# Performance work log

Hardware: AMD Instinct MI355X
Metric: run time of the kernel (lower is better)

The kernel has to match this reference:

```python
import jax, jax.numpy as jnp
import numpy as np

N_NODES = 32768
NUM_EDGES = 524288
NUM_GRAPHS = 32
C = 128            # hidden channels
N_LAYERS = 3       # len(hidden_channels)-1
D_IN = 144         # 4 (op embedding dim) + 140
C_MID = 80         # mem1 out
C_OUT = 64         # mem2 out / classes
H1, K1N = 5, 10    # mem1 heads / clusters
H2, K2N = 5, 1     # mem2 heads / clusters
EPS = 1e-15


def _gatv2(x, src, dst, Wl, bl, Wr, br, att, cb):
    """GATv2Conv (heads=1, negative_slope=0.2), edges src->dst incl. self loops."""
    n = x.shape[0]
    xl = x @ Wl + bl                                  # source transform [N,C]
    xr = x @ Wr + br                                  # target transform [N,C]
    e = (jax.nn.leaky_relu(xl[src] + xr[dst], 0.2) @ att)  # [E]
    m = jax.ops.segment_max(e, dst, num_segments=n)   # segment softmax over in-edges
    ee = jnp.exp(e - m[dst])
    denom = jax.ops.segment_sum(ee, dst, num_segments=n)
    alpha = ee / denom[dst]
    out = jax.ops.segment_sum(alpha[:, None] * xl[src], dst, num_segments=n)
    return out + cb


def _bn(h, gamma, beta):
    # BatchNorm1d with batch statistics (training-mode forward), eps=1e-5
    mu = h.mean(0)
    var = h.var(0)
    return (h - mu) * jax.lax.rsqrt(var + 1e-5) * gamma + beta


def _mem_pool(xd, Kmem, W):
    # xd [B,N,C], Kmem [H,K,C]; Student-t kernel, tau=1 -> (1+d)^-1
    d = (jnp.sum(xd * xd, -1)[:, :, None, None]
         + jnp.sum(Kmem * Kmem, -1)[None, None]
         - 2.0 * jnp.einsum('bnc,hkc->bnhk', xd, Kmem))  # [B,N,H,K] sq. distances
    S = 1.0 / (1.0 + d)
    S = S / S.sum(-1, keepdims=True)   # normalize over clusters
    S = S.mean(2)                      # average heads -> [B,N,K]
    out = jnp.einsum('bnk,bnc->bkc', S, xd) @ W
    return out, S


def _kl_loss(S):
    S2 = S * S / S.sum(1, keepdims=True)
    den = S2.sum(2, keepdims=True)
    den = jnp.where(S.sum(2, keepdims=True) == 0.0, 1.0, den)
    P = jnp.maximum(S2 / den, EPS)
    Sc = jnp.maximum(S, EPS)
    # KLDivLoss(reduction='batchmean'), input = log(S)
    return jnp.sum(P * (jnp.log(P) - jnp.log(Sc))) / S.shape[0]


def setup_inputs():
    key = jax.random.key(0)
    ks = jax.random.split(key, 24)
    x = jax.random.normal(ks[0], (N_NODES, D_IN), jnp.float32)
    edge_index = jax.random.randint(ks[1], (2, NUM_EDGES), 0, N_NODES, jnp.int32)
    batch = (jnp.arange(N_NODES, dtype=jnp.int32) // (N_NODES // NUM_GRAPHS))
    s = 1.0 / np.sqrt(C)
    inp = {
        'x': x, 'edge_index': edge_index, 'batch': batch,
        'W_in': jax.random.normal(ks[2], (D_IN, C), jnp.float32) / np.sqrt(D_IN),
        'b_in': jnp.zeros((C,), jnp.float32),
        'bn_gamma': jnp.ones((N_LAYERS, C), jnp.float32),
        'bn_beta': jnp.zeros((N_LAYERS, C), jnp.float32),
        'Wl': jax.random.normal(ks[3], (N_LAYERS, C, C), jnp.float32) * s,
        'bl': jnp.zeros((N_LAYERS, C), jnp.float32),
        'Wr': jax.random.normal(ks[4], (N_LAYERS, C, C), jnp.float32) * s,
        'br': jnp.zeros((N_LAYERS, C), jnp.float32),
        'att': jax.random.normal(ks[5], (N_LAYERS, C), jnp.float32) * s,
        'conv_bias': jnp.zeros((N_LAYERS, C), jnp.float32),
        'K1': jax.random.normal(ks[6], (H1, K1N, C), jnp.float32),
        'Wm1': jax.random.normal(ks[7], (C, C_MID), jnp.float32) * s,
        'K2': jax.random.normal(ks[8], (H2, K2N, C_MID), jnp.float32),
        'Wm2': jax.random.normal(ks[9], (C_MID, C_OUT), jnp.float32) / np.sqrt(C_MID),
    }
    return inp


def reference(x, edge_index, batch, W_in, b_in, bn_gamma, bn_beta,
              Wl, bl, Wr, br, att, conv_bias, K1, Wm1, K2, Wm2):
    h = x @ W_in + b_in                               # self.linear
    loops = jnp.arange(N_NODES, dtype=edge_index.dtype)
    src = jnp.concatenate([edge_index[0], loops])     # GATv2 add_self_loops=True
    dst = jnp.concatenate([edge_index[1], loops])
    for l in range(N_LAYERS):                         # DeepGCNLayer block='res+'
        t = _bn(h, bn_gamma[l], bn_beta[l])
        t = jax.nn.leaky_relu(t, 0.01)
        # dropout: identity (deterministic reference)
        t = _gatv2(t, src, dst, Wl[l], bl[l], Wr[l], br[l], att[l], conv_bias[l])
        h = h + t
    per = N_NODES // NUM_GRAPHS
    xd = h.reshape(NUM_GRAPHS, per, C)                # to_dense_batch (equal-size graphs)
    x1, S1 = _mem_pool(xd, K1, Wm1)                   # [B,10,80]
    x1 = jax.nn.leaky_relu(x1, 0.01)
    x2, S2 = _mem_pool(x1, K2, Wm2)                   # [B,1,64]
    logits = jax.nn.log_softmax(x2.squeeze(1), -1)    # [B,64]
    return logits, _kl_loss(S1) + _kl_loss(S2)
```

## Files before the change

kernel.cpp:

```cpp
#include <hip/hip_runtime.h>
#include <math.h>

#define N_NODES   32768
#define NUM_EDGES 524288
#define NUM_GRAPHS 32
#define PER_G     1024
#define C         128
#define D_IN      144
#define C_MID     80
#define C_OUT     64
#define NL        3
#define NBINS     32

#define WS_H    0
#define WS_XL   16777216
#define WS_XR   25165824
#define WS_CSR  33554432
#define WS_DEG  35651584
#define WS_CUR  35782656
#define WS_PART 35913728
#define WS_CS   35946496
#define WS_KL   35947776
#define WS_ZERO_BASE WS_DEG
#define WS_ZERO_SIZE (35947780 - 35651584)
#define WS_SC   35948544
#define WS_SH   35949056
#define WS_S1   35949568
#define WS_PP   37260288
#define WS_X1   42503168
#define WS_OFF  42605568

using short8 = __attribute__((ext_vector_type(8))) short;
using f32x4  = __attribute__((ext_vector_type(4))) float;

__device__ __forceinline__ float wave_sum(float v) {
  #pragma unroll
  for (int m = 1; m < 64; m <<= 1) v += __shfl_xor(v, m, 64);
  return v;
}

__device__ __forceinline__ float lrelu2(float v) { return fmaxf(v, 0.2f * v); }

__device__ __forceinline__ unsigned short f2bf(float f) {
  union { float f; unsigned u; } c; c.f = f;
  unsigned r = (c.u + 0x7FFFu + ((c.u >> 16) & 1u)) >> 16;
  return (unsigned short)r;
}
__device__ __forceinline__ float bflo(unsigned u) {
  union { unsigned u; float f; } c; c.u = u << 16; return c.f;
}
__device__ __forceinline__ float bfhi(unsigned u) {
  union { unsigned u; float f; } c; c.u = u & 0xFFFF0000u; return c.f;
}

__global__ void k_count(const int* __restrict__ dst, int* __restrict__ deg) {
  int e = blockIdx.x * 256 + threadIdx.x;
  if (e < NUM_EDGES) atomicAdd(&deg[dst[e]], 1);
}

__global__ __launch_bounds__(1024) void k_scan(const int* __restrict__ deg, int* __restrict__ off) {
  __shared__ int part[1024];
  int t = threadIdx.x;
  int base = t * 32;
  int4 d[8];
  const int4* dp = (const int4*)(deg + base);
  #pragma unroll
  for (int i = 0; i < 8; i++) d[i] = dp[i];
  int s = 0;
  #pragma unroll
  for (int i = 0; i < 8; i++) s += d[i].x + d[i].y + d[i].z + d[i].w;
  part[t] = s;
  __syncthreads();
  for (int dd = 1; dd < 1024; dd <<= 1) {
    int v = (t >= dd) ? part[t - dd] : 0;
    __syncthreads();
    part[t] += v;
    __syncthreads();
  }
  int run = (t == 0) ? 0 : part[t - 1];
  int4* op = (int4*)(off + base);
  #pragma unroll
  for (int i = 0; i < 8; i++) {
    int4 o;
    o.x = run; run += d[i].x;
    o.y = run; run += d[i].y;
    o.z = run; run += d[i].z;
    o.w = run; run += d[i].w;
    op[i] = o;
  }
}

__global__ void k_fill(const int* __restrict__ src, const int* __restrict__ dst,
                       const int* __restrict__ off, int* __restrict__ cur,
                       int* __restrict__ csr) {
  int e = blockIdx.x * 256 + threadIdx.x;
  if (e < NUM_EDGES) {
    int d = dst[e];
    int p = atomicAdd(&cur[d], 1);
    csr[off[d] + p] = src[e];
  }
}

__global__ __launch_bounds__(256) void k_lin_mfma(const float* __restrict__ x,
    const float* __restrict__ W, const float* __restrict__ bias,
    float* __restrict__ h, float* __restrict__ part) {
  __shared__ __align__(16) char smem[61440];
  __shared__ float lsum[128];
  __shared__ float lsum2[128];
  char* tA = smem;
  char* tB = smem + 20480;
  int n0 = blockIdx.x * 64;
  int tid = threadIdx.x;
  if (tid < 128) { lsum[tid] = 0.f; lsum2[tid] = 0.f; }
  for (int t = 0; t < 32; t++) {
    int cp = tid & 127;
    int node = t * 2 + (tid >> 7);
    if (cp < 80) {
      unsigned pkv = 0;
      if (cp < 72) {
        float2 xv = *(const float2*)&x[(size_t)(n0 + node) * D_IN + 2 * cp];
        pkv = ((unsigned)f2bf(xv.y) << 16) | f2bf(xv.x);
      }
      int byte = node * 320 + ((4 * cp) ^ ((node & 3) << 4));
      *(unsigned*)(tA + byte) = pkv;
    }
  }
  {
    int col = tid & 127, hh = tid >> 7;
    for (int t = 0; t < 40; t++) {
      int kp = t * 2 + hh;
      float w0 = (2 * kp < D_IN) ? W[(size_t)(2 * kp) * C + col] : 0.f;
      float w1 = (2 * kp + 1 < D_IN) ? W[(size_t)(2 * kp + 1) * C + col] : 0.f;
      unsigned pkv = ((unsigned)f2bf(w1) << 16) | f2bf(w0);
      int byte = col * 320 + ((4 * kp) ^ ((col & 3) << 4));
      *(unsigned*)(tB + byte) = pkv;
    }
  }
  __syncthreads();
  int l = tid & 63, w = tid >> 6;
  f32x4 acc[8];
  #pragma unroll
  for (int f = 0; f < 8; f++) acc[f] = (f32x4){0.f, 0.f, 0.f, 0.f};
  int arow = w * 16 + (l & 15);
  #pragma unroll
  for (int ks = 0; ks < 5; ks++) {
    int kb = ks * 64 + (l >> 4) * 16;
    short8 a = *(const short8*)(tA + arow * 320 + (kb ^ ((arow & 3) << 4)));
    #pragma unroll
    for (int f = 0; f < 8; f++) {
      int col = f * 16 + (l & 15);
      short8 b = *(const short8*)(tB + col * 320 + (kb ^ ((col & 3) << 4)));
      acc[f] = __builtin_amdgcn_mfma_f32_16x16x32_bf16(a, b, acc[f], 0, 0, 0);
    }
  }
  int rowb = n0 + w * 16 + (l >> 4) * 4;
  #pragma unroll
  for (int f = 0; f < 8; f++) {
    int col = f * 16 + (l & 15);
    float bv = bias[col];
    float s = 0.f, s2 = 0.f;
    #pragma unroll
    for (int r = 0; r < 4; r++) {
      float v = acc[f][r] + bv;
      h[(size_t)(rowb + r) * C + col] = v;
      s += v; s2 += v * v;
    }
    s  += __shfl_xor(s, 16, 64);  s  += __shfl_xor(s, 32, 64);
    s2 += __shfl_xor(s2, 16, 64); s2 += __shfl_xor(s2, 32, 64);
    if (l < 16) {
      atomicAdd(&lsum[col], s);
      atomicAdd(&lsum2[col], s2);
    }
  }
  __syncthreads();
  if (tid < 128) {
    int bin = blockIdx.x & (NBINS - 1);
    atomicAdd(&part[bin * 256 + tid], lsum[tid]);
    atomicAdd(&part[bin * 256 + 128 + tid], lsum2[tid]);
  }
}

__global__ __launch_bounds__(128) void k_bn_part(const float* __restrict__ h, float* __restrict__ part) {
  int b = blockIdx.x; int c = threadIdx.x;
  float s = 0.f, s2 = 0.f;
  int r0 = b * 64;
  for (int r = 0; r < 64; r++) {
    float v = h[(size_t)(r0 + r) * C + c];
    s += v; s2 += v * v;
  }
  int bin = b & (NBINS - 1);
  atomicAdd(&part[bin * 256 + c], s);
  atomicAdd(&part[bin * 256 + 128 + c], s2);
}

__global__ __launch_bounds__(256) void k_bn_fin(float* __restrict__ part,
    const float* __restrict__ gamma, const float* __restrict__ beta,
    float* __restrict__ sc, float* __restrict__ sh) {
  int tid = threadIdx.x;
  if (tid < 128) {
    double S = 0.0, S2 = 0.0;
    for (int b = 0; b < NBINS; b++) {
      S += (double)part[b * 256 + tid];
      S2 += (double)part[b * 256 + 128 + tid];
    }
    double m = S / (double)N_NODES;
    double var = S2 / (double)N_NODES - m * m;
    float rsig = (float)(1.0 / sqrt(var + 1e-5));
    float scv = rsig * gamma[tid];
    sc[tid] = scv;
    sh[tid] = beta[tid] - (float)m * scv;
  }
  __syncthreads();
  for (int i = tid; i < NBINS * 256; i += 256) part[i] = 0.f;
}

__device__ __forceinline__ void gemm_half(const char* tA, const char* tB,
    const float* bias, unsigned short* out, int n0, int tid) {
  int l = tid & 63, w = tid >> 6;
  f32x4 acc[8];
  #pragma unroll
  for (int f = 0; f < 8; f++) acc[f] = (f32x4){0.f, 0.f, 0.f, 0.f};
  int arow = w * 16 + (l & 15);
  #pragma unroll
  for (int ks = 0; ks < 4; ks++) {
    int kb = ks * 64 + (l >> 4) * 16;
    short8 a = *(const short8*)(tA + arow * 256 + (kb ^ ((arow & 7) << 4)));
    #pragma unroll
    for (int f = 0; f < 8; f++) {
      int col = f * 16 + (l & 15);
      short8 b = *(const short8*)(tB + col * 256 + (kb ^ ((col & 7) << 4)));
      acc[f] = __builtin_amdgcn_mfma_f32_16x16x32_bf16(a, b, acc[f], 0, 0, 0);
    }
  }
  int rowb = n0 + w * 16 + (l >> 4) * 4;
  #pragma unroll
  for (int f = 0; f < 8; f++) {
    int col = f * 16 + (l & 15);
    float bv = bias[col];
    #pragma unroll
    for (int r = 0; r < 4; r++)
      out[(size_t)(rowb + r) * C + col] = f2bf(acc[f][r] + bv);
  }
}

__device__ __forceinline__ void stage_B(char* tB, const float* __restrict__ W, int tid) {
  int col = tid & 127, hh = tid >> 7;
  for (int t = 0; t < 32; t++) {
    int kp = t * 2 + hh;
    float w0 = W[(size_t)(2 * kp) * C + col];
    float w1 = W[(size_t)(2 * kp + 1) * C + col];
    unsigned pkv = ((unsigned)f2bf(w1) << 16) | f2bf(w0);
    int byte = col * 256 + ((4 * kp) ^ ((col & 7) << 4));
    *(unsigned*)(tB + byte) = pkv;
  }
}

__global__ __launch_bounds__(256) void k_gemm_mfma(const float* __restrict__ h,
    const float* __restrict__ sc, const float* __restrict__ sh,
    const float* __restrict__ Wl, const float* __restrict__ bl,
    const float* __restrict__ Wr, const float* __restrict__ br,
    unsigned short* __restrict__ xl, unsigned short* __restrict__ xr) {
  __shared__ __align__(16) char smem[49152];
  char* tA = smem;
  char* tB = smem + 16384;
  int n0 = blockIdx.x * 64;
  int tid = threadIdx.x;
  for (int t = 0; t < 16; t++) {
    int item = t * 256 + tid;
    int node = item >> 6;
    int cp = item & 63;
    float2 hv = *(const float2*)&h[(size_t)(n0 + node) * C + 2 * cp];
    float2 scv = *(const float2*)&sc[2 * cp];
    float2 shv = *(const float2*)&sh[2 * cp];
    float t0 = hv.x * scv.x + shv.x; t0 = fmaxf(t0, 0.01f * t0);
    float t1 = hv.y * scv.y + shv.y; t1 = fmaxf(t1, 0.01f * t1);
    unsigned pkv = ((unsigned)f2bf(t1) << 16) | f2bf(t0);
    int byte = node * 256 + ((4 * cp) ^ ((node & 7) << 4));
    *(unsigned*)(tA + byte) = pkv;
  }
  stage_B(tB, Wl, tid);
  __syncthreads();
  gemm_half(tA, tB, bl, xl, n0, tid);
  __syncthreads();
  stage_B(tB, Wr, tid);
  __syncthreads();
  gemm_half(tA, tB, br, xr, n0, tid);
}

#define GAT_EDGE(te, ya, yb, yc, yd)                                       \
  if ((te) > m + 8.f) {                                                    \
    float f_ = __expf(m - (te));                                           \
    ssum = fmaf(ssum, f_, 1.f);                                            \
    acc0 = fmaf(acc0, f_, (ya)); acc1 = fmaf(acc1, f_, (yb));              \
    acc2 = fmaf(acc2, f_, (yc)); acc3 = fmaf(acc3, f_, (yd));              \
    m = (te);                                                              \
  } else {                                                                 \
    float p_ = __expf((te) - m);                                           \
    ssum += p_;                                                            \
    acc0 = fmaf(p_, (ya), acc0); acc1 = fmaf(p_, (yb), acc1);              \
    acc2 = fmaf(p_, (yc), acc2); acc3 = fmaf(p_, (yd), acc3);              \
  }

__global__ __launch_bounds__(256) void k_gat(float* __restrict__ h,
    const unsigned* __restrict__ xlb, const unsigned* __restrict__ xrb,
    const float* __restrict__ att, const float* __restrict__ cb,
    const int* __restrict__ off, const int* __restrict__ deg,
    const int* __restrict__ csr) {
  int tid = threadIdx.x;
  int lane = tid & 63;
  int w = tid >> 6;
  int half = lane >> 5;
  int q = lane & 31;
  int node = blockIdx.x * 8 + w * 2 + half;
  float4 a = *(const float4*)&att[q * 4];
  uint2 ur = *(const uint2*)&xrb[(size_t)node * 64 + q * 2];
  float xr0 = bflo(ur.x), xr1 = bfhi(ur.x), xr2 = bflo(ur.y), xr3 = bfhi(ur.y);
  uint2 us = *(const uint2*)&xlb[(size_t)node * 64 + q * 2];
  float acc0 = bflo(us.x), acc1 = bfhi(us.x), acc2 = bflo(us.y), acc3 = bfhi(us.y);
  float p0 = lrelu2(acc0 + xr0) * a.x + lrelu2(acc1 + xr1) * a.y
           + lrelu2(acc2 + xr2) * a.z + lrelu2(acc3 + xr3) * a.w;
  #pragma unroll
  for (int mm = 1; mm < 32; mm <<= 1) p0 += __shfl_xor(p0, mm, 64);
  float m = p0;
  float ssum = 1.f;
  int o = off[node], dg = deg[node];
  int dgmax = max(dg, __shfl_xor(dg, 32, 64));
  for (int j = 0; j < dgmax; j += 4) {
    int i0 = o + ((j + 0 < dg) ? j + 0 : 0);
    int i1 = o + ((j + 1 < dg) ? j + 1 : 0);
    int i2 = o + ((j + 2 < dg) ? j + 2 : 0);
    int i3 = o + ((j + 3 < dg) ? j + 3 : 0);
    int s0 = csr[i0], s1 = csr[i1], s2 = csr[i2], s3 = csr[i3];
    uint2 u0 = *(const uint2*)&xlb[(size_t)s0 * 64 + q * 2];
    uint2 u1 = *(const uint2*)&xlb[(size_t)s1 * 64 + q * 2];
    uint2 u2 = *(const uint2*)&xlb[(size_t)s2 * 64 + q * 2];
    uint2 u3 = *(const uint2*)&xlb[(size_t)s3 * 64 + q * 2];
    float y00 = bflo(u0.x), y01 = bfhi(u0.x), y02 = bflo(u0.y), y03 = bfhi(u0.y);
    float y10 = bflo(u1.x), y11 = bfhi(u1.x), y12 = bflo(u1.y), y13 = bfhi(u1.y);
    float y20 = bflo(u2.x), y21 = bfhi(u2.x), y22 = bflo(u2.y), y23 = bfhi(u2.y);
    float y30 = bflo(u3.x), y31 = bfhi(u3.x), y32 = bflo(u3.y), y33 = bfhi(u3.y);
    float t0 = lrelu2(y00 + xr0) * a.x + lrelu2(y01 + xr1) * a.y
             + lrelu2(y02 + xr2) * a.z + lrelu2(y03 + xr3) * a.w;
    float t1 = lrelu2(y10 + xr0) * a.x + lrelu2(y11 + xr1) * a.y
             + lrelu2(y12 + xr2) * a.z + lrelu2(y13 + xr3) * a.w;
    float t2 = lrelu2(y20 + xr0) * a.x + lrelu2(y21 + xr1) * a.y
             + lrelu2(y22 + xr2) * a.z + lrelu2(y23 + xr3) * a.w;
    float t3 = lrelu2(y30 + xr0) * a.x + lrelu2(y31 + xr1) * a.y
             + lrelu2(y32 + xr2) * a.z + lrelu2(y33 + xr3) * a.w;
    #pragma unroll
    for (int mm = 1; mm < 32; mm <<= 1) {
      t0 += __shfl_xor(t0, mm, 64);
      t1 += __shfl_xor(t1, mm, 64);
      t2 += __shfl_xor(t2, mm, 64);
      t3 += __shfl_xor(t3, mm, 64);
    }
    t0 = (j + 0 < dg) ? t0 : -1e30f;
    t1 = (j + 1 < dg) ? t1 : -1e30f;
    t2 = (j + 2 < dg) ? t2 : -1e30f;
    t3 = (j + 3 < dg) ? t3 : -1e30f;
    GAT_EDGE(t0, y00, y01, y02, y03);
    GAT_EDGE(t1, y10, y11, y12, y13);
    GAT_EDGE(t2, y20, y21, y22, y23);
    GAT_EDGE(t3, y30, y31, y32, y33);
  }
  float inv = 1.f / ssum;
  float4 cbv = *(const float4*)&cb[q * 4];
  float4 hv = *(float4*)&h[(size_t)node * C + q * 4];
  hv.x += acc0 * inv + cbv.x;
  hv.y += acc1 * inv + cbv.y;
  hv.z += acc2 * inv + cbv.z;
  hv.w += acc3 * inv + cbv.w;
  *(float4*)&h[(size_t)node * C + q * 4] = hv;
}

__global__ __launch_bounds__(320) void k_mem1(const float* __restrict__ h,
    const float* __restrict__ K1, float* __restrict__ S1, float* __restrict__ colsum) {
  __shared__ float dd[64 * 51];
  __shared__ float kn[50];
  int tid = threadIdx.x;
  int lane = tid & 63;
  int w = tid >> 6;
  int n0 = blockIdx.x * 64;
  if (tid < 50) {
    const float4* kr = reinterpret_cast<const float4*>(K1 + tid * C);
    float s = 0.f;
    for (int q = 0; q < 32; q++) {
      float4 kv = kr[q];
      s += kv.x * kv.x + kv.y * kv.y + kv.z * kv.z + kv.w * kv.w;
    }
    kn[tid] = s;
  }
  int wu = __builtin_amdgcn_readfirstlane(w);
  const float4* x4 = reinterpret_cast<const float4*>(h + (size_t)(n0 + lane) * C);
  const float4* K4 = reinterpret_cast<const float4*>(K1);
  float acc[10];
  #pragma unroll
  for (int it = 0; it < 10; it++) acc[it] = 0.f;
  float xn = 0.f;
  for (int q = 0; q < 32; q += 2) {
    float4 xa = x4[q], xb = x4[q + 1];
    xn += xa.x * xa.x + xa.y * xa.y + xa.z * xa.z + xa.w * xa.w
        + xb.x * xb.x + xb.y * xb.y + xb.z * xb.z + xb.w * xb.w;
    #pragma unroll
    for (int it = 0; it < 10; it++) {
      int j = wu + 5 * it;
      float4 ka = K4[j * 32 + q], kb = K4[j * 32 + q + 1];
      acc[it] += xa.x * ka.x + xa.y * ka.y + xa.z * ka.z + xa.w * ka.w
               + xb.x * kb.x + xb.y * kb.y + xb.z * kb.z + xb.w * kb.w;
    }
  }
  #pragma unroll
  for (int it = 0; it < 10; it++) dd[lane * 51 + wu + 5 * it] = acc[it];
  __syncthreads();
  if (tid < 64) {
    float sn[10];
    #pragma unroll
    for (int k = 0; k < 10; k++) sn[k] = 0.f;
    #pragma unroll
    for (int hd = 0; hd < 5; hd++) {
      float sh_[10]; float hs = 0.f;
      #pragma unroll
      for (int k = 0; k < 10; k++) {
        int j = hd * 10 + k;
        float dist = xn + kn[j] - 2.f * dd[tid * 51 + j];
        float s = 1.f / (1.f + dist);
        sh_[k] = s; hs += s;
      }
      float inv = 1.f / hs;
      #pragma unroll
      for (int k = 0; k < 10; k++) sn[k] += sh_[k] * inv;
    }
    int b = n0 >> 10;
    #pragma unroll
    for (int k = 0; k < 10; k++) {
      float v = 0.2f * sn[k];
      S1[(n0 + tid) * 10 + k] = v;
      float vs = wave_sum(v);
      if (tid == 0) atomicAdd(&colsum[b * 10 + k], vs);
    }
  }
}

__global__ __launch_bounds__(128) void k_pool1a(const float* __restrict__ h,
    const float* __restrict__ S1, float* __restrict__ pp) {
  int b = blockIdx.x >> 5, ch = blockIdx.x & 31;
  int c = threadIdx.x;
  float acc[10];
  #pragma unroll
  for (int k = 0; k < 10; k++) acc[k] = 0.f;
  int n0 = ch * 32;
  for (int n = 0; n < 32; n++) {
    int i = b * PER_G + n0 + n;
    float xv = h[(size_t)i * C + c];
    #pragma unroll
    for (int k = 0; k < 10; k++) acc[k] += S1[i * 10 + k] * xv;
  }
  #pragma unroll
  for (int k = 0; k < 10; k++) pp[(size_t)((b * 32 + ch) * 10 + k) * C + c] = acc[k];
}

__global__ __launch_bounds__(128) void k_pool1b(const float* __restrict__ pp,
    const float* __restrict__ Wm1, float* __restrict__ x1) {
  int bk = blockIdx.x; int b = bk / 10; int k = bk - b * 10;
  int c = threadIdx.x;
  __shared__ float red[C];
  float r = 0.f;
  for (int ch = 0; ch < 32; ch++) r += pp[(size_t)((b * 32 + ch) * 10 + k) * C + c];
  red[c] = r;
  __syncthreads();
  if (c < C_MID) {
    float o = 0.f;
    for (int mIdx = 0; mIdx < C; mIdx++) o += red[mIdx] * Wm1[mIdx * C_MID + c];
    o = fmaxf(o, 0.01f * o);
    x1[bk * C_MID + c] = o;
  }
}

__global__ __launch_bounds__(256) void k_kl1(const float* __restrict__ S1,
    const float* __restrict__ colsum, float* __restrict__ kl) {
  int i = blockIdx.x * 256 + threadIdx.x;
  int b = i >> 10;
  float s[10], q[10];
  float den = 0.f;
  #pragma unroll
  for (int k = 0; k < 10; k++) {
    s[k] = S1[i * 10 + k];
    q[k] = s[k] * s[k] / colsum[b * 10 + k];
    den += q[k];
  }
  float inv = 1.f / den;
  float term = 0.f;
  #pragma unroll
  for (int k = 0; k < 10; k++) {
    float P = fmaxf(q[k] * inv, 1e-15f);
    float Sc = fmaxf(s[k], 1e-15f);
    term += P * (logf(P) - logf(Sc));
  }
  term *= (1.f / (float)NUM_GRAPHS);
  term = wave_sum(term);
  if ((threadIdx.x & 63) == 0) atomicAdd(kl, term);
}

__global__ __launch_bounds__(128) void k_mem2(const float* __restrict__ x1,
    const float* __restrict__ Wm2, const float* __restrict__ kl, float* __restrict__ out) {
  int b = blockIdx.x;
  __shared__ float t80[C_MID];
  int tid = threadIdx.x;
  if (tid < C_MID) {
    float s = 0.f;
    #pragma unroll
    for (int k = 0; k < 10; k++) s += x1[(b * 10 + k) * C_MID + tid];
    t80[tid] = s;
  }
  __syncthreads();
  if (tid < C_OUT) {
    float o = 0.f;
    for (int mIdx = 0; mIdx < C_MID; mIdx++) o += t80[mIdx] * Wm2[mIdx * C_OUT + tid];
    float mx = o;
    #pragma unroll
    for (int d = 1; d < 64; d <<= 1) mx = fmaxf(mx, __shfl_xor(mx, d, 64));
    float p = expf(o - mx);
    float sum = p;
    #pragma unroll
    for (int d = 1; d < 64; d <<= 1) sum += __shfl_xor(sum, d, 64);
    out[b * C_OUT + tid] = o - mx - logf(sum);
  }
  if (b == 0 && tid == 127) out[NUM_GRAPHS * C_OUT] = kl[0];
}

extern "C" void kernel_launch(void* const* d_in, const int* in_sizes, int n_in,
                              void* d_out, int out_size, void* d_ws, size_t ws_size,
                              hipStream_t stream) {
  const float* x    = (const float*)d_in[0];
  const int*   ei   = (const int*)d_in[1];
  const float* W_in = (const float*)d_in[3];
  const float* b_in = (const float*)d_in[4];
  const float* bn_g = (const float*)d_in[5];
  const float* bn_b = (const float*)d_in[6];
  const float* Wl   = (const float*)d_in[7];
  const float* bl   = (const float*)d_in[8];
  const float* Wr   = (const float*)d_in[9];
  const float* br   = (const float*)d_in[10];
  const float* att  = (const float*)d_in[11];
  const float* cb   = (const float*)d_in[12];
  const float* K1   = (const float*)d_in[13];
  const float* Wm1  = (const float*)d_in[14];
  const float* Wm2  = (const float*)d_in[16];
  float* out = (float*)d_out;

  char* ws = (char*)d_ws;
  float* h    = (float*)(ws + WS_H);
  unsigned short* xlp = (unsigned short*)(ws + WS_XL);
  unsigned short* xrp = (unsigned short*)(ws + WS_XR);
  int*   csr  = (int*)(ws + WS_CSR);
  int*   deg  = (int*)(ws + WS_DEG);
  int*   off  = (int*)(ws + WS_OFF);
  int*   cur  = (int*)(ws + WS_CUR);
  float* part = (float*)(ws + WS_PART);
  float* scv  = (float*)(ws + WS_SC);
  float* shv  = (float*)(ws + WS_SH);
  float* S1p  = (float*)(ws + WS_S1);
  float* cs   = (float*)(ws + WS_CS);
  float* pp   = (float*)(ws + WS_PP);
  float* x1p  = (float*)(ws + WS_X1);
  float* klp  = (float*)(ws + WS_KL);

  const int* srcp = ei;
  const int* dstp = ei + NUM_EDGES;

  hipMemsetAsync(ws + WS_ZERO_BASE, 0, WS_ZERO_SIZE, stream);

  k_count<<<NUM_EDGES / 256, 256, 0, stream>>>(dstp, deg);
  k_scan<<<1, 1024, 0, stream>>>(deg, off);
  k_fill<<<NUM_EDGES / 256, 256, 0, stream>>>(srcp, dstp, off, cur, csr);

  k_lin_mfma<<<N_NODES / 64, 256, 0, stream>>>(x, W_in, b_in, h, part);

  for (int l = 0; l < NL; l++) {
    if (l > 0) k_bn_part<<<N_NODES / 64, 128, 0, stream>>>(h, part);
    k_bn_fin<<<1, 256, 0, stream>>>(part, bn_g + l * C, bn_b + l * C, scv, shv);
    k_gemm_mfma<<<N_NODES / 64, 256, 0, stream>>>(h, scv, shv,
        Wl + l * C * C, bl + l * C,
        Wr + l * C * C, br + l * C,
        xlp, xrp);
    k_gat<<<N_NODES / 8, 256, 0, stream>>>(h, (const unsigned*)xlp, (const unsigned*)xrp,
        att + l * C, cb + l * C, off, deg, csr);
  }

  k_mem1<<<N_NODES / 64, 320, 0, stream>>>(h, K1, S1p, cs);
  k_pool1a<<<NUM_GRAPHS * 32, 128, 0, stream>>>(h, S1p, pp);
  k_pool1b<<<NUM_GRAPHS * 10, 128, 0, stream>>>(pp, Wm1, x1p);
  k_kl1<<<N_NODES / 256, 256, 0, stream>>>(S1p, cs, klp);
  k_mem2<<<NUM_GRAPHS, 128, 0, stream>>>(x1p, Wm2, klp, out);
}
```

Baseline: 303.5 us.

## Pre-pack bf16 swizzled weights once and vectorize GEMM tile staging

Adds a prep kernel that converts W_in, Wl and Wr to bf16 in the swizzled shared-memory layout once per call, so each GEMM block copies the B tile with 16-byte loads instead of re-converting strided fp32 weights. The A-tile staging in the input linear now uses float4 loads with a changed swizzle, and the GEMM A staging batches its loads before converting. This removes redundant per-block weight conversion in exchange for one extra small launch and more workspace.

```diff
diff --git a/kernel.cpp b/kernel.cpp
--- a/kernel.cpp
+++ b/kernel.cpp
@@ -29,6 +29,8 @@
 #define WS_PP   37260288
 #define WS_X1   42503168
 #define WS_OFF  42605568
+#define WS_WINT 42736640
+#define WS_WLRT 42777600
 
 using short8 = __attribute__((ext_vector_type(8))) short;
 using f32x4  = __attribute__((ext_vector_type(4))) float;
@@ -101,8 +103,54 @@
   }
 }
 
+__global__ __launch_bounds__(256) void k_prep(const float* __restrict__ W_in,
+    const float* __restrict__ Wl, const float* __restrict__ Wr,
+    char* __restrict__ winT, char* __restrict__ wlrT) {
+  int bid = blockIdx.x;
+  int tid = threadIdx.x;
+  int col = tid & 127, hh = tid >> 7;
+  if (bid < 4) {
+    int q = bid;
+    float w0[10], w1[10];
+    #pragma unroll
+    for (int i = 0; i < 10; i++) {
+      int p = 2 * (q * 10 + i) + hh;
+      w0[i] = (2 * p < D_IN) ? W_in[(size_t)(2 * p) * C + col] : 0.f;
+      w1[i] = (2 * p + 1 < D_IN) ? W_in[(size_t)(2 * p + 1) * C + col] : 0.f;
+    }
+    #pragma unroll
+    for (int i = 0; i < 10; i++) {
+      int p = 2 * (q * 10 + i) + hh;
+      unsigned pkv = ((unsigned)f2bf(w1[i]) << 16) | f2bf(w0[i]);
+      int byte = col * 320 + ((4 * p) ^ (((col >> 1) & 3) << 4));
+      *(unsigned*)(winT + byte) = pkv;
+    }
+  } else {
+    int id = bid - 4;
+    int m = id >> 2;
+    int q = id & 3;
+    int l = m >> 1, r = m & 1;
+    const float* W = (r ? Wr : Wl) + (size_t)l * C * C;
+    char* dst = wlrT + (size_t)m * 32768;
+    float w0[8], w1[8];
+    #pragma unroll
+    for (int i = 0; i < 8; i++) {
+      int p = 2 * (q * 8 + i) + hh;
+      w0[i] = W[(size_t)(2 * p) * C + col];
+      w1[i] = W[(size_t)(2 * p + 1) * C + col];
+    }
+    #pragma unroll
+    for (int i = 0; i < 8; i++) {
+      int p = 2 * (q * 8 + i) + hh;
+      unsigned pkv = ((unsigned)f2bf(w1[i]) << 16) | f2bf(w0[i]);
+      int byte = col * 256 + ((4 * p) ^ ((col & 7) << 4));
+      *(unsigned*)(dst + byte) = pkv;
+    }
+  }
+}
+
 __global__ __launch_bounds__(256) void k_lin_mfma(const float* __restrict__ x,
-    const float* __restrict__ W, const float* __restrict__ bias,
+    const char* __restrict__ winT, const float* __restrict__ bias,
     float* __restrict__ h, float* __restrict__ part) {
   __shared__ __align__(16) char smem[61440];
   __shared__ float lsum[128];
@@ -112,29 +160,34 @@
   int n0 = blockIdx.x * 64;
   int tid = threadIdx.x;
   if (tid < 128) { lsum[tid] = 0.f; lsum2[tid] = 0.f; }
-  for (int t = 0; t < 32; t++) {
-    int cp = tid & 127;
-    int node = t * 2 + (tid >> 7);
-    if (cp < 80) {
-      unsigned pkv = 0;
-      if (cp < 72) {
-        float2 xv = *(const float2*)&x[(size_t)(n0 + node) * D_IN + 2 * cp];
-        pkv = ((unsigned)f2bf(xv.y) << 16) | f2bf(xv.x);
-      }
-      int byte = node * 320 + ((4 * cp) ^ ((node & 3) << 4));
-      *(unsigned*)(tA + byte) = pkv;
-    }
-  }
   {
-    int col = tid & 127, hh = tid >> 7;
-    for (int t = 0; t < 40; t++) {
-      int kp = t * 2 + hh;
-      float w0 = (2 * kp < D_IN) ? W[(size_t)(2 * kp) * C + col] : 0.f;
-      float w1 = (2 * kp + 1 < D_IN) ? W[(size_t)(2 * kp + 1) * C + col] : 0.f;
-      unsigned pkv = ((unsigned)f2bf(w1) << 16) | f2bf(w0);
-      int byte = col * 320 + ((4 * kp) ^ ((col & 3) << 4));
-      *(unsigned*)(tB + byte) = pkv;
-    }
+    float4 xv[10];
+    #pragma unroll
+    for (int k = 0; k < 10; k++) {
+      int idx = k * 256 + tid;
+      int row = idx / 40, j = idx - row * 40;
+      xv[k] = (j < 36) ? *(const float4*)&x[(size_t)(n0 + row) * D_IN + 4 * j]
+                       : (float4){0.f, 0.f, 0.f, 0.f};
+    }
+    #pragma unroll
+    for (int k = 0; k < 10; k++) {
+      int idx = k * 256 + tid;
+      int row = idx / 40, j = idx - row * 40;
+      uint2 pk;
+      pk.x = ((unsigned)f2bf(xv[k].y) << 16) | f2bf(xv[k].x);
+      pk.y = ((unsigned)f2bf(xv[k].w) << 16) | f2bf(xv[k].z);
+      int byte = row * 320 + ((8 * j) ^ (((row >> 1) & 3) << 4));
+      *(uint2*)(tA + byte) = pk;
+    }
+  }
+  {
+    const uint4* src = (const uint4*)winT;
+    uint4* d = (uint4*)tB;
+    uint4 v[10];
+    #pragma unroll
+    for (int k = 0; k < 10; k++) v[k] = src[k * 256 + tid];
+    #pragma unroll
+    for (int k = 0; k < 10; k++) d[k * 256 + tid] = v[k];
   }
   __syncthreads();
   int l = tid & 63, w = tid >> 6;
@@ -145,11 +198,11 @@
   #pragma unroll
   for (int ks = 0; ks < 5; ks++) {
     int kb = ks * 64 + (l >> 4) * 16;
-    short8 a = *(const short8*)(tA + arow * 320 + (kb ^ ((arow & 3) << 4)));
+    short8 a = *(const short8*)(tA + arow * 320 + (kb ^ (((arow >> 1) & 3) << 4)));
     #pragma unroll
     for (int f = 0; f < 8; f++) {
       int col = f * 16 + (l & 15);
-      short8 b = *(const short8*)(tB + col * 320 + (kb ^ ((col & 3) << 4)));
+      short8 b = *(const short8*)(tB + col * 320 + (kb ^ (((col >> 1) & 3) << 4)));
       acc[f] = __builtin_amdgcn_mfma_f32_16x16x32_bf16(a, b, acc[f], 0, 0, 0);
     }
   }
@@ -243,46 +296,49 @@
   }
 }
 
-__device__ __forceinline__ void stage_B(char* tB, const float* __restrict__ W, int tid) {
-  int col = tid & 127, hh = tid >> 7;
-  for (int t = 0; t < 32; t++) {
-    int kp = t * 2 + hh;
-    float w0 = W[(size_t)(2 * kp) * C + col];
-    float w1 = W[(size_t)(2 * kp + 1) * C + col];
-    unsigned pkv = ((unsigned)f2bf(w1) << 16) | f2bf(w0);
-    int byte = col * 256 + ((4 * kp) ^ ((col & 7) << 4));
-    *(unsigned*)(tB + byte) = pkv;
-  }
+__device__ __forceinline__ void copy_B(char* tB, const char* __restrict__ WT, int tid) {
+  const uint4* src = (const uint4*)WT;
+  uint4* d = (uint4*)tB;
+  uint4 v[8];
+  #pragma unroll
+  for (int k = 0; k < 8; k++) v[k] = src[k * 256 + tid];
+  #pragma unroll
+  for (int k = 0; k < 8; k++) d[k * 256 + tid] = v[k];
 }
 
 __global__ __launch_bounds__(256) void k_gemm_mfma(const float* __restrict__ h,
     const float* __restrict__ sc, const float* __restrict__ sh,
-    const float* __restrict__ Wl, const float* __restrict__ bl,
-    const float* __restrict__ Wr, const float* __restrict__ br,
+    const char* __restrict__ WlT, const float* __restrict__ bl,
+    const char* __restrict__ WrT, const float* __restrict__ br,
     unsigned short* __restrict__ xl, unsigned short* __restrict__ xr) {
   __shared__ __align__(16) char smem[49152];
   char* tA = smem;
   char* tB = smem + 16384;
   int n0 = blockIdx.x * 64;
   int tid = threadIdx.x;
-  for (int t = 0; t < 16; t++) {
-    int item = t * 256 + tid;
-    int node = item >> 6;
-    int cp = item & 63;
-    float2 hv = *(const float2*)&h[(size_t)(n0 + node) * C + 2 * cp];
+  {
+    int cp = tid & 63, w4 = tid >> 6;
     float2 scv = *(const float2*)&sc[2 * cp];
     float2 shv = *(const float2*)&sh[2 * cp];
-    float t0 = hv.x * scv.x + shv.x; t0 = fmaxf(t0, 0.01f * t0);
-    float t1 = hv.y * scv.y + shv.y; t1 = fmaxf(t1, 0.01f * t1);
-    unsigned pkv = ((unsigned)f2bf(t1) << 16) | f2bf(t0);
-    int byte = node * 256 + ((4 * cp) ^ ((node & 7) << 4));
-    *(unsigned*)(tA + byte) = pkv;
-  }
-  stage_B(tB, Wl, tid);
+    float2 hv[16];
+    #pragma unroll
+    for (int t = 0; t < 16; t++)
+      hv[t] = *(const float2*)&h[(size_t)(n0 + t * 4 + w4) * C + 2 * cp];
+    #pragma unroll
+    for (int t = 0; t < 16; t++) {
+      int node = t * 4 + w4;
+      float t0 = hv[t].x * scv.x + shv.x; t0 = fmaxf(t0, 0.01f * t0);
+      float t1 = hv[t].y * scv.y + shv.y; t1 = fmaxf(t1, 0.01f * t1);
+      unsigned pkv = ((unsigned)f2bf(t1) << 16) | f2bf(t0);
+      int byte = node * 256 + ((4 * cp) ^ ((node & 7) << 4));
+      *(unsigned*)(tA + byte) = pkv;
+    }
+  }
+  copy_B(tB, WlT, tid);
   __syncthreads();
   gemm_half(tA, tB, bl, xl, n0, tid);
   __syncthreads();
-  stage_B(tB, Wr, tid);
+  copy_B(tB, WrT, tid);
   __syncthreads();
   gemm_half(tA, tB, br, xr, n0, tid);
 }
@@ -564,24 +620,27 @@
   float* pp   = (float*)(ws + WS_PP);
   float* x1p  = (float*)(ws + WS_X1);
   float* klp  = (float*)(ws + WS_KL);
+  char*  winT = ws + WS_WINT;
+  char*  wlrT = ws + WS_WLRT;
 
   const int* srcp = ei;
   const int* dstp = ei + NUM_EDGES;
 
   hipMemsetAsync(ws + WS_ZERO_BASE, 0, WS_ZERO_SIZE, stream);
 
+  k_prep<<<28, 256, 0, stream>>>(W_in, Wl, Wr, winT, wlrT);
   k_count<<<NUM_EDGES / 256, 256, 0, stream>>>(dstp, deg);
   k_scan<<<1, 1024, 0, stream>>>(deg, off);
   k_fill<<<NUM_EDGES / 256, 256, 0, stream>>>(srcp, dstp, off, cur, csr);
 
-  k_lin_mfma<<<N_NODES / 64, 256, 0, stream>>>(x, W_in, b_in, h, part);
+  k_lin_mfma<<<N_NODES / 64, 256, 0, stream>>>(x, winT, b_in, h, part);
 
   for (int l = 0; l < NL; l++) {
     if (l > 0) k_bn_part<<<N_NODES / 64, 128, 0, stream>>>(h, part);
     k_bn_fin<<<1, 256, 0, stream>>>(part, bn_g + l * C, bn_b + l * C, scv, shv);
     k_gemm_mfma<<<N_NODES / 64, 256, 0, stream>>>(h, scv, shv,
-        Wl + l * C * C, bl + l * C,
-        Wr + l * C * C, br + l * C,
+        wlrT + (size_t)(l * 2) * 32768, bl + l * C,
+        wlrT + (size_t)(l * 2 + 1) * 32768, br + l * C,
         xlp, xrp);
     k_gat<<<N_NODES / 8, 256, 0, stream>>>(h, (const unsigned*)xlp, (const unsigned*)xrp,
         att + l * C, cb + l * C, off, deg, csr);
```

After: 284.3 us. 1.07x faster.
